# Optimization experiments

Hardware: AMD Instinct MI355X
Metric: run time of the kernel (lower is better)

Reference implementation:

```python
import jax, jax.numpy as jnp
import numpy as np

B, N, D, H, HID, EN = 2, 4096, 128, 4, 32, 16
ALPHA = 0.2           # LeakyReLU slope
NEG = -9e15           # masked_fill value from the original code


def setup_inputs() -> dict:
    key = jax.random.key(0)
    ks = jax.random.split(key, 6)
    fea = jax.random.normal(ks[0], (B, N, D), dtype=jnp.float32)
    # binary dense adjacency (regulon x gene), square here so narrow() is identity
    adj = jax.random.randint(ks[1], (B, N, N), 0, 2).astype(jnp.float32)
    # per-head GAT params (xavier-ish scale)
    W_heads = jax.random.normal(ks[2], (H, D, HID), dtype=jnp.float32) * 0.1
    a_heads = jax.random.normal(ks[3], (H, 2 * HID, 1), dtype=jnp.float32) * 0.1
    W_last = jax.random.normal(ks[4], (H * HID, EN), dtype=jnp.float32) * 0.1
    a_last = jax.random.normal(ks[5], (2 * EN, 1), dtype=jnp.float32) * 0.1
    return {"fea_mats": fea, "adj_mats": adj, "W_heads": W_heads,
            "a_heads": a_heads, "W_last": W_last, "a_last": a_last}


def _gat_layer(x, adj, W, a, concat):
    # x: [N, d_in], adj: [nr, N], W: [d_in, out], a: [2*out, 1]
    out_dim = W.shape[1]
    wh = x @ W                                   # [N, out]
    nr = adj.shape[0]
    wh1 = wh[:nr] @ a[:out_dim]                  # [nr, 1]
    wh2 = wh @ a[out_dim:]                       # [N, 1]
    e = jax.nn.leaky_relu(wh1 + wh2.T, ALPHA)    # [nr, N]
    # _prepare_attentions: mask by adj, weight by adj, fill zeros with -9e15
    att = jnp.where(adj != 0, e * adj, 0.0)
    att = jnp.where(att == 0, NEG, att)
    att = jax.nn.softmax(att, axis=1)
    # the original detaches attention via a numpy roundtrip
    att = jax.lax.stop_gradient(att)
    res = att @ wh                               # [nr, out]
    return jax.nn.elu(res) if concat else res


def reference(fea_mats, adj_mats, W_heads, a_heads, W_last, a_last):
    def per_sample(x, adj):
        # multi-head attention layers (concat=True), vmapped over heads
        heads = jax.vmap(lambda W, a: _gat_layer(x, adj, W, a, True))(W_heads, a_heads)  # [H, N, HID]
        xcat = jnp.transpose(heads, (1, 0, 2)).reshape(x.shape[0], H * HID)  # torch.cat(dim=1)
        nr = adj.shape[0]
        out = _gat_layer(xcat, adj[:, :nr], W_last, a_last, False)  # adj.narrow(1,0,nr)
        return jax.nn.elu(out)  # [N, EN]
    return jax.vmap(per_sample)(fea_mats, adj_mats)  # [B, N, EN]
```

## Files before the change

kernel.cpp:

```cpp
#include <hip/hip_runtime.h>
#include <hip/hip_bf16.h>
#include <stdint.h>

#define B_ 2
#define N_ 4096
#define D_ 128
#define H_ 4
#define HID_ 32
#define EN_ 16
#define ALPHA_ 0.2f
#define S1_ 4
#define S2_ 4
#define LOG2E_ 1.4426950408889634f

typedef __attribute__((ext_vector_type(8))) _Float16 f16x8;
typedef __attribute__((ext_vector_type(4))) float f32x4;
typedef __attribute__((ext_vector_type(8))) unsigned short u16x8;

__device__ __forceinline__ unsigned short f2h(float v) {
    _Float16 h = (_Float16)v;
    return *(unsigned short*)&h;
}

__global__ __launch_bounds__(256) void prep_kernel(
    const float* __restrict__ adj, unsigned long long* __restrict__ mask,
    const float* __restrict__ fea, const float* __restrict__ Wh,
    const float* __restrict__ a_heads,
    float* __restrict__ wh1, float* __restrict__ wh2,
    float* __restrict__ cmax1, unsigned short* __restrict__ whTt)
{
    __shared__ float xs[32][132];
    __shared__ float WT[32][132];
    __shared__ float Wa[2][128];
    __shared__ float as_[2 * HID_];
    __shared__ unsigned short ts[32][32];
    __shared__ float rmax[32];
    const int tid = threadIdx.x;

    if (blockIdx.x < 2048) {
        const int b = blockIdx.x >> 10, ib = blockIdx.x & 1023;
        const int i = ib * 4 + (tid >> 6);
        const int lane = tid & 63;
        const float* ar = adj + ((size_t)b * N_ + i) * N_;
        unsigned long long* mrow = mask + ((size_t)b * N_ + i) * 64;
#pragma unroll 4
        for (int c = 0; c < 16; ++c) {
            float4 v = *(const float4*)(ar + c * 256 + lane * 4);
            unsigned long long b0 = __ballot(v.x != 0.f);
            unsigned long long b1 = __ballot(v.y != 0.f);
            unsigned long long b2 = __ballot(v.z != 0.f);
            unsigned long long b3 = __ballot(v.w != 0.f);
            if (lane == 0) {
                ulonglong2 w01 = {b0, b1}, w23 = {b2, b3};
                *(ulonglong2*)(mrow + c * 4) = w01;
                *(ulonglong2*)(mrow + c * 4 + 2) = w23;
            }
        }
        return;
    }
    const int l0 = blockIdx.x - 2048;
    const int ib = l0 & 127, h = (l0 >> 7) & 3, b = l0 >> 9;
    const int i0 = ib * 32;
    const float* Wp = Wh + (size_t)h * D_ * HID_;
    for (int l = tid; l < 1024; l += 256) {
        float4 w4 = *(const float4*)(Wp + l * 4);
        int k = l >> 3, d = (l & 7) * 4;
        WT[d][k] = w4.x; WT[d + 1][k] = w4.y; WT[d + 2][k] = w4.z; WT[d + 3][k] = w4.w;
    }
    if (tid < 2 * HID_) as_[tid] = a_heads[h * 2 * HID_ + tid];
    const float* xp = fea + ((size_t)b * N_ + i0) * D_;
    for (int l = tid; l < 1024; l += 256) {
        int r = l >> 5, k4 = (l & 31) * 4;
        *(float4*)&xs[r][k4] = *(const float4*)(xp + r * D_ + k4);
    }
    __syncthreads();
    {
        const int k = tid & 127, j = tid >> 7;
        const float* wr = Wp + k * HID_;
        const float* aw = &as_[j * HID_];
        float s = 0.f;
#pragma unroll
        for (int d = 0; d < HID_; d += 4) {
            float4 w4 = *(const float4*)(wr + d);
            s += w4.x * aw[d] + w4.y * aw[d + 1] + w4.z * aw[d + 2] + w4.w * aw[d + 3];
        }
        Wa[j][k] = s;
    }
    const int c = tid & 15, rg = (tid >> 4) * 2;
    float a0[2] = {0.f, 0.f}, a1[2] = {0.f, 0.f};
#pragma unroll 8
    for (int k = 0; k < D_; k += 4) {
        float4 w0 = *(float4*)&WT[c][k];
        float4 w1 = *(float4*)&WT[c + 16][k];
#pragma unroll
        for (int i = 0; i < 2; ++i) {
            float4 x4 = *(float4*)&xs[rg + i][k];
            a0[i] += x4.x * w0.x + x4.y * w0.y + x4.z * w0.z + x4.w * w0.w;
            a1[i] += x4.x * w1.x + x4.y * w1.y + x4.z * w1.z + x4.w * w1.w;
        }
    }
#pragma unroll
    for (int i = 0; i < 2; ++i) {
        ts[c][rg + i] = f2h(a0[i]);
        ts[c + 16][rg + i] = f2h(a1[i]);
    }
    __syncthreads();
    {
        const int row = tid >> 3, q = tid & 7;
        float d1 = 0.f, d2 = 0.f;
#pragma unroll
        for (int k = q * 16; k < q * 16 + 16; k += 4) {
            float4 x4 = *(float4*)&xs[row][k];
            float4 u = *(float4*)&Wa[0][k];
            float4 v = *(float4*)&Wa[1][k];
            d1 += x4.x * u.x + x4.y * u.y + x4.z * u.z + x4.w * u.w;
            d2 += x4.x * v.x + x4.y * v.y + x4.z * v.z + x4.w * v.w;
        }
        d1 += __shfl_xor(d1, 1); d1 += __shfl_xor(d1, 2); d1 += __shfl_xor(d1, 4);
        d2 += __shfl_xor(d2, 1); d2 += __shfl_xor(d2, 2); d2 += __shfl_xor(d2, 4);
        if (q == 0) {
            const size_t o = (size_t)(b * H_ + h) * N_ + i0 + row;
            wh1[o] = d1 * LOG2E_;
            wh2[o] = d2 * LOG2E_;
            rmax[row] = d2 * LOG2E_;
        }
    }
    __syncthreads();
    if (tid < 128) {
        const int d = tid >> 2, part = (tid & 3) * 8;
        unsigned short* dst = whTt + ((size_t)(b * H_ + h) * 64 + (i0 >> 6)) * 2048
                            + d * 64 + (i0 & 63) + part;
        *(u16x8*)dst = *(u16x8*)&ts[d][part];
    }
    if (tid < 32) {
        float mx = rmax[tid];
#pragma unroll
        for (int off = 16; off; off >>= 1) mx = fmaxf(mx, __shfl_xor(mx, off));
        if (tid == 0) cmax1[(size_t)(b * H_ + h) * 128 + ib] = mx;
    }
}

__global__ __launch_bounds__(256, 4) void attn1_kernel(
    const unsigned long long* __restrict__ mask, const unsigned short* __restrict__ whT,
    const float* __restrict__ wh1, const float* __restrict__ wh2,
    const float* __restrict__ cmax1,
    float* __restrict__ x2p, float* __restrict__ l1p)
{
    __shared__ unsigned long long mask_s[32][17];
    const int b = blockIdx.z, split = blockIdx.y, i0 = blockIdx.x * 32;
    const int tid = threadIdx.x, lane = tid & 63, h = tid >> 6;
    const int m = lane & 15, quad = lane >> 4;
    {
        const int r = tid >> 3, w = (tid & 7) * 2;
        ulonglong2 mw = *(const ulonglong2*)(mask + ((size_t)b * N_ + i0 + r) * 64
                                             + split * 16 + w);
        mask_s[r][w] = mw.x; mask_s[r][w + 1] = mw.y;
    }
    const float* cm = cmax1 + (size_t)(b * H_ + h) * 128;
    float Mh = fmaxf(cm[lane], cm[lane + 64]);
#pragma unroll
    for (int off = 32; off; off >>= 1) Mh = fmaxf(Mh, __shfl_xor(Mh, off));
    const size_t bhN = (size_t)(b * H_ + h) * N_;
    const float w1r0 = wh1[bhN + i0 + m];
    const float w1r1 = wh1[bhN + i0 + 16 + m];
    const float sb0 = w1r0 + Mh, sb1 = w1r1 + Mh;
    const float mr0 = fmaxf(sb0, ALPHA_ * sb0);
    const float mr1 = fmaxf(sb1, ALPHA_ * sb1);
    const float* wvb = wh2 + bhN + split * 1024 + quad * 8;
    const unsigned short* bpb = whT + (size_t)(b * H_ + h) * 131072
                              + (size_t)split * 16 * 2048 + m * 64 + quad * 8;
    f32x4 a00 = {0.f,0.f,0.f,0.f}, a01 = {0.f,0.f,0.f,0.f}, a02 = {0.f,0.f,0.f,0.f};
    f32x4 a10 = {0.f,0.f,0.f,0.f}, a11 = {0.f,0.f,0.f,0.f}, a12 = {0.f,0.f,0.f,0.f};
    f16x8 ones;
#pragma unroll
    for (int q = 0; q < 8; ++q) ones[q] = (_Float16)1.0f;
    __syncthreads();

    for (int c = 0; c < 4; ++c) {
        const unsigned long long P0 = mask_s[m][c*4+0], P1 = mask_s[m][c*4+1];
        const unsigned long long P2 = mask_s[m][c*4+2], P3 = mask_s[m][c*4+3];
        const unsigned long long Q0 = mask_s[m+16][c*4+0], Q1 = mask_s[m+16][c*4+1];
        const unsigned long long Q2 = mask_s[m+16][c*4+2], Q3 = mask_s[m+16][c*4+3];
#pragma unroll
        for (int q4 = 0; q4 < 4; ++q4) {
            const int t = c * 4 + q4;
            const unsigned short* bp = bpb + (size_t)t * 2048;
            f16x8 b00 = *(const f16x8*)bp;
            f16x8 b10 = *(const f16x8*)(bp + 32);
            f16x8 b01 = *(const f16x8*)(bp + 1024);
            f16x8 b11 = *(const f16x8*)(bp + 1056);
            const float* nw = wvb + t * 64;
            float4 u0 = *(const float4*)nw;
            float4 u1 = *(const float4*)(nw + 4);
            float4 v0 = *(const float4*)(nw + 32);
            float4 v1 = *(const float4*)(nw + 36);
#pragma unroll
            for (int ks = 0; ks < 2; ++ks) {
                const int sh = 16 * q4 + 8 * ks + 2 * quad;
                float wv8[8];
                if (ks == 0) { *(float4*)&wv8[0] = u0; *(float4*)&wv8[4] = u1; }
                else         { *(float4*)&wv8[0] = v0; *(float4*)&wv8[4] = v1; }
                const unsigned int gp0 = (unsigned int)(P0 >> sh) & 3u;
                const unsigned int gp1 = (unsigned int)(P1 >> sh) & 3u;
                const unsigned int gp2 = (unsigned int)(P2 >> sh) & 3u;
                const unsigned int gp3 = (unsigned int)(P3 >> sh) & 3u;
                const unsigned int gq0 = (unsigned int)(Q0 >> sh) & 3u;
                const unsigned int gq1 = (unsigned int)(Q1 >> sh) & 3u;
                const unsigned int gq2 = (unsigned int)(Q2 >> sh) & 3u;
                const unsigned int gq3 = (unsigned int)(Q3 >> sh) & 3u;
                f16x8 af0, af1;
#pragma unroll
                for (int qq = 0; qq < 4; ++qq) {
                    float r0p[2], r1p[2];
#pragma unroll
                    for (int cc = 0; cc < 2; ++cc) {
                        const int jj = qq * 2 + cc;
                        const unsigned int bsel = 1u << (jj >> 2);
                        const unsigned int gp = (jj&3)==0?gp0:(jj&3)==1?gp1:(jj&3)==2?gp2:gp3;
                        const unsigned int gq = (jj&3)==0?gq0:(jj&3)==1?gq1:(jj&3)==2?gq2:gq3;
                        float s0 = w1r0 + wv8[jj];
                        float e0 = fmaxf(s0, ALPHA_ * s0);
                        float t0 = ((gp & bsel) == 0u || s0 == 0.f) ? -1e38f : (e0 - mr0);
                        r0p[cc] = __builtin_amdgcn_exp2f(t0);
                        float s1 = w1r1 + wv8[jj];
                        float e1 = fmaxf(s1, ALPHA_ * s1);
                        float t1 = ((gq & bsel) == 0u || s1 == 0.f) ? -1e38f : (e1 - mr1);
                        r1p[cc] = __builtin_amdgcn_exp2f(t1);
                    }
                    auto pr0 = __builtin_amdgcn_cvt_pkrtz(r0p[0], r0p[1]);
                    af0[qq*2] = (_Float16)pr0[0]; af0[qq*2+1] = (_Float16)pr0[1];
                    auto pr1 = __builtin_amdgcn_cvt_pkrtz(r1p[0], r1p[1]);
                    af1[qq*2] = (_Float16)pr1[0]; af1[qq*2+1] = (_Float16)pr1[1];
                }
                f16x8 bb0 = ks ? b10 : b00;
                f16x8 bb1 = ks ? b11 : b01;
                a00 = __builtin_amdgcn_mfma_f32_16x16x32_f16(af0, bb0, a00, 0, 0, 0);
                a01 = __builtin_amdgcn_mfma_f32_16x16x32_f16(af0, bb1, a01, 0, 0, 0);
                a02 = __builtin_amdgcn_mfma_f32_16x16x32_f16(af0, ones, a02, 0, 0, 0);
                a10 = __builtin_amdgcn_mfma_f32_16x16x32_f16(af1, bb0, a10, 0, 0, 0);
                a11 = __builtin_amdgcn_mfma_f32_16x16x32_f16(af1, bb1, a11, 0, 0, 0);
                a12 = __builtin_amdgcn_mfma_f32_16x16x32_f16(af1, ones, a12, 0, 0, 0);
            }
        }
    }
    float* xp = x2p + (((size_t)split * B_ + b) * N_ + i0) * D_ + h * HID_;
#pragma unroll
    for (int reg = 0; reg < 4; ++reg) {
        const int row = quad * 4 + reg;
        xp[(size_t)row * D_ + m] = a00[reg];
        xp[(size_t)row * D_ + 16 + m] = a01[reg];
        xp[(size_t)(row + 16) * D_ + m] = a10[reg];
        xp[(size_t)(row + 16) * D_ + 16 + m] = a11[reg];
    }
    if (m == 0) {
        float* lp = l1p + (((size_t)split * B_ + b) * N_ + i0) * H_ + h;
#pragma unroll
        for (int reg = 0; reg < 4; ++reg) {
            lp[(size_t)(quad * 4 + reg) * H_] = a02[reg];
            lp[(size_t)(quad * 4 + reg + 16) * H_] = a12[reg];
        }
    }
}

__global__ __launch_bounds__(256) void proj2_kernel(
    const float* __restrict__ x2p, const float* __restrict__ l1p,
    const float* __restrict__ Wl, const float* __restrict__ a_last,
    float* __restrict__ wh1b, float* __restrict__ wh2b,
    float* __restrict__ cmax2, unsigned short* __restrict__ whT2t)
{
    __shared__ float Ws[D_ * EN_];
    __shared__ float xs[16][D_];
    __shared__ float as_[2 * EN_];
    __shared__ unsigned short ts[EN_][16];
    __shared__ float rmax[16];
    const int b = blockIdx.y, i0 = blockIdx.x * 16, tid = threadIdx.x;
    for (int idx = tid * 4; idx < D_ * EN_; idx += 1024)
        *(float4*)&Ws[idx] = *(const float4*)(Wl + idx);
    if (tid < 2 * EN_) as_[tid] = a_last[tid];
    for (int idx = tid * 4; idx < 16 * D_; idx += 1024) {
        const int r = idx >> 7, hd = idx & 127, h = hd >> 5;
        float4 v = {0.f, 0.f, 0.f, 0.f};
        float l = 0.f;
#pragma unroll
        for (int s = 0; s < S1_; ++s) {
            const size_t gi = ((size_t)s * B_ + b) * N_ + i0 + r;
            float4 p = *(const float4*)(x2p + gi * D_ + hd);
            v.x += p.x; v.y += p.y; v.z += p.z; v.w += p.w;
            l += l1p[gi * H_ + h];
        }
        float linv = 1.f / fmaxf(l, 1e-30f);
        float o0 = v.x * linv, o1 = v.y * linv, o2 = v.z * linv, o3 = v.w * linv;
        xs[r][hd]     = o0 > 0.f ? o0 : expm1f(o0);
        xs[r][hd + 1] = o1 > 0.f ? o1 : expm1f(o1);
        xs[r][hd + 2] = o2 > 0.f ? o2 : expm1f(o2);
        xs[r][hd + 3] = o3 > 0.f ? o3 : expm1f(o3);
    }
    __syncthreads();
    const int r = tid >> 4, e = tid & 15;
    float acc = 0.f;
#pragma unroll 8
    for (int k = 0; k < D_; ++k) acc += xs[r][k] * Ws[k * EN_ + e];
    ts[e][r] = f2h(acc);
    float d1 = acc * as_[e], d2 = acc * as_[EN_ + e];
#pragma unroll
    for (int off = 8; off; off >>= 1) {
        d1 += __shfl_xor(d1, off);
        d2 += __shfl_xor(d2, off);
    }
    d1 *= LOG2E_; d2 *= LOG2E_;
    if (e == 0) {
        wh1b[(size_t)b * N_ + i0 + r] = d1;
        wh2b[(size_t)b * N_ + i0 + r] = d2;
        rmax[r] = d2;
    }
    __syncthreads();
    if (tid < EN_) {
        unsigned short* dst = whT2t + (size_t)b * 65536
                            + (i0 >> 6) * 1024 + tid * 64 + (i0 & 63);
        *(u16x8*)dst = *(u16x8*)&ts[tid][0];
        *(u16x8*)(dst + 8) = *(u16x8*)&ts[tid][8];
    }
    if (tid == 0) {
        float mx = rmax[0];
#pragma unroll
        for (int k = 1; k < 16; ++k) mx = fmaxf(mx, rmax[k]);
        cmax2[(size_t)b * 256 + blockIdx.x] = mx;
    }
}

__global__ __launch_bounds__(256, 4) void attn2_kernel(
    const unsigned long long* __restrict__ mask, const unsigned short* __restrict__ whT2,
    const float* __restrict__ wh1b, const float* __restrict__ wh2b,
    const float* __restrict__ cmax2,
    float* __restrict__ outp, float* __restrict__ outlp)
{
    __shared__ unsigned long long mask_s[32][17];
    __shared__ float accred[4][32][17];
    __shared__ float lred[4][32];
    const int b = blockIdx.z, split = blockIdx.y, i0 = blockIdx.x * 32;
    const int tid = threadIdx.x, lane = tid & 63, wv = tid >> 6;
    const int m = lane & 15, quad = lane >> 4;
    {
        const int r = tid >> 3, w = (tid & 7) * 2;
        ulonglong2 mw = *(const ulonglong2*)(mask + ((size_t)b * N_ + i0 + r) * 64
                                             + split * 16 + w);
        mask_s[r][w] = mw.x; mask_s[r][w + 1] = mw.y;
    }
    const float* cm = cmax2 + (size_t)b * 256;
    float4 c0 = *(const float4*)(cm + lane * 4);
    float Mh = fmaxf(fmaxf(c0.x, c0.y), fmaxf(c0.z, c0.w));
#pragma unroll
    for (int off = 32; off; off >>= 1) Mh = fmaxf(Mh, __shfl_xor(Mh, off));
    const float w1r0 = wh1b[(size_t)b * N_ + i0 + m];
    const float w1r1 = wh1b[(size_t)b * N_ + i0 + 16 + m];
    const float sb0 = w1r0 + Mh, sb1 = w1r1 + Mh;
    const float mr0 = fmaxf(sb0, ALPHA_ * sb0);
    const float mr1 = fmaxf(sb1, ALPHA_ * sb1);
    const unsigned short* wTb = whT2 + (size_t)b * 65536
                              + (size_t)(split * 16 + wv * 4) * 1024 + m * 64 + quad * 8;
    const float* wvb = wh2b + (size_t)b * N_ + split * 1024 + wv * 256 + quad * 8;
    f32x4 a0 = {0.f,0.f,0.f,0.f}, a1 = {0.f,0.f,0.f,0.f};
    f32x4 l0 = {0.f,0.f,0.f,0.f}, l1 = {0.f,0.f,0.f,0.f};
    f16x8 ones;
#pragma unroll
    for (int q = 0; q < 8; ++q) ones[q] = (_Float16)1.0f;
    __syncthreads();
    const unsigned long long P0 = mask_s[m][wv*4+0], P1 = mask_s[m][wv*4+1];
    const unsigned long long P2 = mask_s[m][wv*4+2], P3 = mask_s[m][wv*4+3];
    const unsigned long long Q0 = mask_s[m+16][wv*4+0], Q1 = mask_s[m+16][wv*4+1];
    const unsigned long long Q2 = mask_s[m+16][wv*4+2], Q3 = mask_s[m+16][wv*4+3];
#pragma unroll
    for (int q4 = 0; q4 < 4; ++q4) {
        const unsigned short* bp = wTb + (size_t)q4 * 1024;
        f16x8 cb0 = *(const f16x8*)(bp);
        f16x8 cb1 = *(const f16x8*)(bp + 32);
        const float* nw = wvb + q4 * 64;
        float4 u0 = *(const float4*)(nw);
        float4 u1 = *(const float4*)(nw + 4);
        float4 v0 = *(const float4*)(nw + 32);
        float4 v1 = *(const float4*)(nw + 36);
#pragma unroll
        for (int ks = 0; ks < 2; ++ks) {
            const int sh = 16 * q4 + 8 * ks + 2 * quad;
            float wv8[8];
            if (ks == 0) { *(float4*)&wv8[0] = u0; *(float4*)&wv8[4] = u1; }
            else         { *(float4*)&wv8[0] = v0; *(float4*)&wv8[4] = v1; }
            const unsigned int gp0 = (unsigned int)(P0 >> sh) & 3u;
            const unsigned int gp1 = (unsigned int)(P1 >> sh) & 3u;
            const unsigned int gp2 = (unsigned int)(P2 >> sh) & 3u;
            const unsigned int gp3 = (unsigned int)(P3 >> sh) & 3u;
            const unsigned int gq0 = (unsigned int)(Q0 >> sh) & 3u;
            const unsigned int gq1 = (unsigned int)(Q1 >> sh) & 3u;
            const unsigned int gq2 = (unsigned int)(Q2 >> sh) & 3u;
            const unsigned int gq3 = (unsigned int)(Q3 >> sh) & 3u;
            f16x8 af0, af1;
#pragma unroll
            for (int qq = 0; qq < 4; ++qq) {
                float r0p[2], r1p[2];
#pragma unroll
                for (int cc = 0; cc < 2; ++cc) {
                    const int jj = qq * 2 + cc;
                    const unsigned int bsel = 1u << (jj >> 2);
                    const unsigned int gp = (jj&3)==0?gp0:(jj&3)==1?gp1:(jj&3)==2?gp2:gp3;
                    const unsigned int gq = (jj&3)==0?gq0:(jj&3)==1?gq1:(jj&3)==2?gq2:gq3;
                    float s0 = w1r0 + wv8[jj];
                    float e0 = fmaxf(s0, ALPHA_ * s0);
                    float t0 = ((gp & bsel) == 0u || s0 == 0.f) ? -1e38f : (e0 - mr0);
                    r0p[cc] = __builtin_amdgcn_exp2f(t0);
                    float s1 = w1r1 + wv8[jj];
                    float e1 = fmaxf(s1, ALPHA_ * s1);
                    float t1 = ((gq & bsel) == 0u || s1 == 0.f) ? -1e38f : (e1 - mr1);
                    r1p[cc] = __builtin_amdgcn_exp2f(t1);
                }
                auto pr0 = __builtin_amdgcn_cvt_pkrtz(r0p[0], r0p[1]);
                af0[qq*2] = (_Float16)pr0[0]; af0[qq*2+1] = (_Float16)pr0[1];
                auto pr1 = __builtin_amdgcn_cvt_pkrtz(r1p[0], r1p[1]);
                af1[qq*2] = (_Float16)pr1[0]; af1[qq*2+1] = (_Float16)pr1[1];
            }
            f16x8 bb = ks ? cb1 : cb0;
            a0 = __builtin_amdgcn_mfma_f32_16x16x32_f16(af0, bb, a0, 0, 0, 0);
            l0 = __builtin_amdgcn_mfma_f32_16x16x32_f16(af0, ones, l0, 0, 0, 0);
            a1 = __builtin_amdgcn_mfma_f32_16x16x32_f16(af1, bb, a1, 0, 0, 0);
            l1 = __builtin_amdgcn_mfma_f32_16x16x32_f16(af1, ones, l1, 0, 0, 0);
        }
    }
#pragma unroll
    for (int reg = 0; reg < 4; ++reg) {
        accred[wv][quad * 4 + reg][m] = a0[reg];
        accred[wv][quad * 4 + reg + 16][m] = a1[reg];
    }
    if (m == 0) {
#pragma unroll
        for (int reg = 0; reg < 4; ++reg) {
            lred[wv][quad * 4 + reg] = l0[reg];
            lred[wv][quad * 4 + reg + 16] = l1[reg];
        }
    }
    __syncthreads();
    const int row = tid >> 4, col = tid & 15;
    float s0 = accred[0][row][col] + accred[1][row][col]
             + accred[2][row][col] + accred[3][row][col];
    float s1 = accred[0][row + 16][col] + accred[1][row + 16][col]
             + accred[2][row + 16][col] + accred[3][row + 16][col];
    float* op = outp + (((size_t)split * B_ + b) * N_ + i0) * EN_;
    op[(size_t)row * EN_ + col] = s0;
    op[(size_t)(row + 16) * EN_ + col] = s1;
    if (tid < 32) {
        float l = lred[0][tid] + lred[1][tid] + lred[2][tid] + lred[3][tid];
        outlp[((size_t)split * B_ + b) * N_ + i0 + tid] = l;
    }
}

__global__ __launch_bounds__(256) void finalize2_kernel(
    const float* __restrict__ outp, const float* __restrict__ outlp,
    float* __restrict__ out)
{
    const int id = blockIdx.x * 256 + threadIdx.x;
    const int gi = id >> 4;
    float num = 0.f, l = 0.f;
#pragma unroll
    for (int s = 0; s < S2_; ++s) {
        num += outp[(size_t)s * B_ * N_ * EN_ + id];
        l   += outlp[(size_t)s * B_ * N_ + gi];
    }
    float v = num / fmaxf(l, 1e-30f);
    out[id] = v > 0.f ? v : expm1f(v);
}

extern "C" void kernel_launch(void* const* d_in, const int* in_sizes, int n_in,
                              void* d_out, int out_size, void* d_ws, size_t ws_size,
                              hipStream_t stream)
{
    const float* fea = (const float*)d_in[0];
    const float* adj = (const float*)d_in[1];
    const float* Wh  = (const float*)d_in[2];
    const float* ah  = (const float*)d_in[3];
    const float* Wl  = (const float*)d_in[4];
    const float* al  = (const float*)d_in[5];

    float* p = (float*)d_ws;
    float* wh1   = p;  p += (size_t)B_ * H_ * N_;
    float* wh2   = p;  p += (size_t)B_ * H_ * N_;
    float* wh1b  = p;  p += (size_t)B_ * N_;
    float* wh2b  = p;  p += (size_t)B_ * N_;
    float* cmax1 = p;  p += (size_t)B_ * H_ * 128;
    float* cmax2 = p;  p += (size_t)B_ * 256;
    float* l1p   = p;  p += (size_t)S1_ * B_ * N_ * H_;
    float* x2p   = p;  p += (size_t)S1_ * B_ * N_ * D_;
    float* outp  = p;  p += (size_t)S2_ * B_ * N_ * EN_;
    float* outlp = p;  p += (size_t)S2_ * B_ * N_;
    unsigned long long* mask = (unsigned long long*)p;
    unsigned short* whTt  = (unsigned short*)(mask + (size_t)B_ * N_ * 64);
    unsigned short* whT2t = whTt + (size_t)B_ * H_ * 131072;

    prep_kernel<<<2048 + B_ * H_ * 128, 256, 0, stream>>>(adj, mask, fea, Wh, ah,
                                                          wh1, wh2, cmax1, whTt);
    attn1_kernel<<<dim3(N_ / 32, S1_, B_), 256, 0, stream>>>(mask, whTt, wh1, wh2, cmax1,
                                                             x2p, l1p);
    proj2_kernel<<<dim3(N_ / 16, B_), 256, 0, stream>>>(x2p, l1p, Wl, al,
                                                        wh1b, wh2b, cmax2, whT2t);
    attn2_kernel<<<dim3(N_ / 32, S2_, B_), 256, 0, stream>>>(mask, whT2t, wh1b, wh2b, cmax2,
                                                             outp, outlp);
    finalize2_kernel<<<(B_ * N_ * EN_) / 256, 256, 0, stream>>>(outp, outlp, (float*)d_out);
}
```

Baseline: 283.6 us.

## Factor attention exponentials into per-row and per-column precomputed tables

Rewrites exp2(leaky(w1+w2) - mr) as a product of a per-row factor and a per-column factor, choosing the positive or negative branch by comparing w2 against -w1. Per-column exp values for both branches are computed once per block into shared memory, and per-row factors once per thread. This replaces the transcendental in the inner loop with a multiply and select plus LDS reads. It costs extra shared memory (32KB in attn1), which may lower occupancy, and adds some rounding differences from the factored exponent.

```diff
diff --git a/kernel.cpp b/kernel.cpp
--- a/kernel.cpp
+++ b/kernel.cpp
@@ -147,6 +147,7 @@
     float* __restrict__ x2p, float* __restrict__ l1p)
 {
     __shared__ unsigned long long mask_s[32][17];
+    __shared__ float Btab[H_][2][1024];
     const int b = blockIdx.z, split = blockIdx.y, i0 = blockIdx.x * 32;
     const int tid = threadIdx.x, lane = tid & 63, h = tid >> 6;
     const int m = lane & 15, quad = lane >> 4;
@@ -161,11 +162,32 @@
 #pragma unroll
     for (int off = 32; off; off >>= 1) Mh = fmaxf(Mh, __shfl_xor(Mh, off));
     const size_t bhN = (size_t)(b * H_ + h) * N_;
+    const float* w2g = wh2 + bhN + split * 1024;
+#pragma unroll
+    for (int g = 0; g < 4; ++g) {
+        float4 v = *(const float4*)(w2g + g * 256 + lane * 4);
+        float4 eb, ep;
+        eb.x = __builtin_amdgcn_exp2f(v.x - Mh);
+        eb.y = __builtin_amdgcn_exp2f(v.y - Mh);
+        eb.z = __builtin_amdgcn_exp2f(v.z - Mh);
+        eb.w = __builtin_amdgcn_exp2f(v.w - Mh);
+        ep.x = __builtin_amdgcn_exp2f(ALPHA_ * (v.x - Mh));
+        ep.y = __builtin_amdgcn_exp2f(ALPHA_ * (v.y - Mh));
+        ep.z = __builtin_amdgcn_exp2f(ALPHA_ * (v.z - Mh));
+        ep.w = __builtin_amdgcn_exp2f(ALPHA_ * (v.w - Mh));
+        *(float4*)&Btab[h][0][g * 256 + lane * 4] = eb;
+        *(float4*)&Btab[h][1][g * 256 + lane * 4] = ep;
+    }
     const float w1r0 = wh1[bhN + i0 + m];
     const float w1r1 = wh1[bhN + i0 + 16 + m];
     const float sb0 = w1r0 + Mh, sb1 = w1r1 + Mh;
     const float mr0 = fmaxf(sb0, ALPHA_ * sb0);
     const float mr1 = fmaxf(sb1, ALPHA_ * sb1);
+    const float th0 = -w1r0, th1 = -w1r1;
+    const float Fp0 = __builtin_amdgcn_exp2f(sb0 - mr0);
+    const float Fn0 = __builtin_amdgcn_exp2f(ALPHA_ * sb0 - mr0);
+    const float Fp1 = __builtin_amdgcn_exp2f(sb1 - mr1);
+    const float Fn1 = __builtin_amdgcn_exp2f(ALPHA_ * sb1 - mr1);
     const float* wvb = wh2 + bhN + split * 1024 + quad * 8;
     const unsigned short* bpb = whT + (size_t)(b * H_ + h) * 131072
                               + (size_t)split * 16 * 2048 + m * 64 + quad * 8;
@@ -200,6 +222,15 @@
                 float wv8[8];
                 if (ks == 0) { *(float4*)&wv8[0] = u0; *(float4*)&wv8[4] = u1; }
                 else         { *(float4*)&wv8[0] = v0; *(float4*)&wv8[4] = v1; }
+                float Bj[8], Bp8[8];
+                {
+                    const float* Bb = &Btab[h][0][t * 64 + ks * 32 + quad * 8];
+                    const float* Pb = &Btab[h][1][t * 64 + ks * 32 + quad * 8];
+                    *(float4*)&Bj[0]  = *(const float4*)Bb;
+                    *(float4*)&Bj[4]  = *(const float4*)(Bb + 4);
+                    *(float4*)&Bp8[0] = *(const float4*)Pb;
+                    *(float4*)&Bp8[4] = *(const float4*)(Pb + 4);
+                }
                 const unsigned int gp0 = (unsigned int)(P0 >> sh) & 3u;
                 const unsigned int gp1 = (unsigned int)(P1 >> sh) & 3u;
                 const unsigned int gp2 = (unsigned int)(P2 >> sh) & 3u;
@@ -218,14 +249,11 @@
                         const unsigned int bsel = 1u << (jj >> 2);
                         const unsigned int gp = (jj&3)==0?gp0:(jj&3)==1?gp1:(jj&3)==2?gp2:gp3;
                         const unsigned int gq = (jj&3)==0?gq0:(jj&3)==1?gq1:(jj&3)==2?gq2:gq3;
-                        float s0 = w1r0 + wv8[jj];
-                        float e0 = fmaxf(s0, ALPHA_ * s0);
-                        float t0 = ((gp & bsel) == 0u || s0 == 0.f) ? -1e38f : (e0 - mr0);
-                        r0p[cc] = __builtin_amdgcn_exp2f(t0);
-                        float s1 = w1r1 + wv8[jj];
-                        float e1 = fmaxf(s1, ALPHA_ * s1);
-                        float t1 = ((gq & bsel) == 0u || s1 == 0.f) ? -1e38f : (e1 - mr1);
-                        r1p[cc] = __builtin_amdgcn_exp2f(t1);
+                        const float w2v = wv8[jj];
+                        float v0s = (w2v > th0) ? Fp0 * Bj[jj] : Fn0 * Bp8[jj];
+                        r0p[cc] = ((gp & bsel) == 0u || w2v == th0) ? 0.f : v0s;
+                        float v1s = (w2v > th1) ? Fp1 * Bj[jj] : Fn1 * Bp8[jj];
+                        r1p[cc] = ((gq & bsel) == 0u || w2v == th1) ? 0.f : v1s;
                     }
                     auto pr0 = __builtin_amdgcn_cvt_pkrtz(r0p[0], r0p[1]);
                     af0[qq*2] = (_Float16)pr0[0]; af0[qq*2+1] = (_Float16)pr0[1];
@@ -337,6 +365,7 @@
     __shared__ unsigned long long mask_s[32][17];
     __shared__ float accred[4][32][17];
     __shared__ float lred[4][32];
+    __shared__ float Btab2[2][1024];
     const int b = blockIdx.z, split = blockIdx.y, i0 = blockIdx.x * 32;
     const int tid = threadIdx.x, lane = tid & 63, wv = tid >> 6;
     const int m = lane & 15, quad = lane >> 4;
@@ -351,11 +380,30 @@
     float Mh = fmaxf(fmaxf(c0.x, c0.y), fmaxf(c0.z, c0.w));
 #pragma unroll
     for (int off = 32; off; off >>= 1) Mh = fmaxf(Mh, __shfl_xor(Mh, off));
+    {
+        float4 v = *(const float4*)(wh2b + (size_t)b * N_ + split * 1024 + tid * 4);
+        float4 eb, ep;
+        eb.x = __builtin_amdgcn_exp2f(v.x - Mh);
+        eb.y = __builtin_amdgcn_exp2f(v.y - Mh);
+        eb.z = __builtin_amdgcn_exp2f(v.z - Mh);
+        eb.w = __builtin_amdgcn_exp2f(v.w - Mh);
+        ep.x = __builtin_amdgcn_exp2f(ALPHA_ * (v.x - Mh));
+        ep.y = __builtin_amdgcn_exp2f(ALPHA_ * (v.y - Mh));
+        ep.z = __builtin_amdgcn_exp2f(ALPHA_ * (v.z - Mh));
+        ep.w = __builtin_amdgcn_exp2f(ALPHA_ * (v.w - Mh));
+        *(float4*)&Btab2[0][tid * 4] = eb;
+        *(float4*)&Btab2[1][tid * 4] = ep;
+    }
     const float w1r0 = wh1b[(size_t)b * N_ + i0 + m];
     const float w1r1 = wh1b[(size_t)b * N_ + i0 + 16 + m];
     const float sb0 = w1r0 + Mh, sb1 = w1r1 + Mh;
     const float mr0 = fmaxf(sb0, ALPHA_ * sb0);
     const float mr1 = fmaxf(sb1, ALPHA_ * sb1);
+    const float th0 = -w1r0, th1 = -w1r1;
+    const float Fp0 = __builtin_amdgcn_exp2f(sb0 - mr0);
+    const float Fn0 = __builtin_amdgcn_exp2f(ALPHA_ * sb0 - mr0);
+    const float Fp1 = __builtin_amdgcn_exp2f(sb1 - mr1);
+    const float Fn1 = __builtin_amdgcn_exp2f(ALPHA_ * sb1 - mr1);
     const unsigned short* wTb = whT2 + (size_t)b * 65536
                               + (size_t)(split * 16 + wv * 4) * 1024 + m * 64 + quad * 8;
     const float* wvb = wh2b + (size_t)b * N_ + split * 1024 + wv * 256 + quad * 8;
@@ -385,6 +433,15 @@
             float wv8[8];
             if (ks == 0) { *(float4*)&wv8[0] = u0; *(float4*)&wv8[4] = u1; }
             else         { *(float4*)&wv8[0] = v0; *(float4*)&wv8[4] = v1; }
+            float Bj[8], Bp8[8];
+            {
+                const float* Bb = &Btab2[0][wv * 256 + q4 * 64 + ks * 32 + quad * 8];
+                const float* Pb = &Btab2[1][wv * 256 + q4 * 64 + ks * 32 + quad * 8];
+                *(float4*)&Bj[0]  = *(const float4*)Bb;
+                *(float4*)&Bj[4]  = *(const float4*)(Bb + 4);
+                *(float4*)&Bp8[0] = *(const float4*)Pb;
+                *(float4*)&Bp8[4] = *(const float4*)(Pb + 4);
+            }
             const unsigned int gp0 = (unsigned int)(P0 >> sh) & 3u;
             const unsigned int gp1 = (unsigned int)(P1 >> sh) & 3u;
             const unsigned int gp2 = (unsigned int)(P2 >> sh) & 3u;
@@ -403,14 +460,11 @@
                     const unsigned int bsel = 1u << (jj >> 2);
                     const unsigned int gp = (jj&3)==0?gp0:(jj&3)==1?gp1:(jj&3)==2?gp2:gp3;
                     const unsigned int gq = (jj&3)==0?gq0:(jj&3)==1?gq1:(jj&3)==2?gq2:gq3;
-                    float s0 = w1r0 + wv8[jj];
-                    float e0 = fmaxf(s0, ALPHA_ * s0);
-                    float t0 = ((gp & bsel) == 0u || s0 == 0.f) ? -1e38f : (e0 - mr0);
-                    r0p[cc] = __builtin_amdgcn_exp2f(t0);
-                    float s1 = w1r1 + wv8[jj];
-                    float e1 = fmaxf(s1, ALPHA_ * s1);
-                    float t1 = ((gq & bsel) == 0u || s1 == 0.f) ? -1e38f : (e1 - mr1);
-                    r1p[cc] = __builtin_amdgcn_exp2f(t1);
+                    const float w2v = wv8[jj];
+                    float v0s = (w2v > th0) ? Fp0 * Bj[jj] : Fn0 * Bp8[jj];
+                    r0p[cc] = ((gp & bsel) == 0u || w2v == th0) ? 0.f : v0s;
+                    float v1s = (w2v > th1) ? Fp1 * Bj[jj] : Fn1 * Bp8[jj];
+                    r1p[cc] = ((gq & bsel) == 0u || w2v == th1) ? 0.f : v1s;
                 }
                 auto pr0 = __builtin_amdgcn_cvt_pkrtz(r0p[0], r0p[1]);
                 af0[qq*2] = (_Float16)pr0[0]; af0[qq*2+1] = (_Float16)pr0[1];
```

Result: no change. 278.2 us (-1.9%).
